# Optimization experiments

Hardware: AMD Instinct MI355X
Metric: run time of the kernel (lower is better)

The kernel has to match this reference:

```python
import jax, jax.numpy as jnp
import numpy as np

N_NODES = 20000
N_EDGES = 640000
IN_DIM = 128
HID_DIM = 256
N_CLASSES = 3
N_TYPES = 4
N_ASPECTS = 4096


def _type_aware_gcn(x, W_type, W_self, b, src, dst, etypes, n_nodes):
    # Per-node, per-type transforms: [N, T, H]
    xt = jnp.einsum('nd,tdh->nth', x, W_type)
    # Per-edge message: transform of source node under the edge's type. [E, H]
    msg = xt[src, etypes]
    # Degree-normalized scatter-sum into destination nodes.
    agg = jax.ops.segment_sum(msg, dst, num_segments=n_nodes)
    deg = jax.ops.segment_sum(jnp.ones((src.shape[0],), dtype=x.dtype), dst,
                              num_segments=n_nodes)
    agg = agg / jnp.clip(deg, 1.0)[:, None]
    # Self-loop transform + bias.
    return agg + x @ W_self + b


def setup_inputs() -> dict:
    key = jax.random.key(0)
    ks = jax.random.split(key, 12)
    features = jax.random.normal(ks[0], (N_NODES, IN_DIM), dtype=jnp.float32)
    edge_index = jax.random.randint(ks[1], (2, N_EDGES), 0, N_NODES)
    edge_types = jax.random.randint(ks[2], (N_EDGES,), 0, N_TYPES)
    aspect_indices = jax.random.randint(ks[3], (N_ASPECTS,), 0, N_NODES)
    s1 = 1.0 / np.sqrt(IN_DIM)
    s2 = 1.0 / np.sqrt(HID_DIM)
    W_type1 = jax.random.uniform(ks[4], (N_TYPES, IN_DIM, HID_DIM), minval=-s1, maxval=s1)
    W_self1 = jax.random.uniform(ks[5], (IN_DIM, HID_DIM), minval=-s1, maxval=s1)
    b1 = jnp.zeros((HID_DIM,), dtype=jnp.float32)
    W_type2 = jax.random.uniform(ks[6], (N_TYPES, HID_DIM, HID_DIM), minval=-s2, maxval=s2)
    W_self2 = jax.random.uniform(ks[7], (HID_DIM, HID_DIM), minval=-s2, maxval=s2)
    b2 = jnp.zeros((HID_DIM,), dtype=jnp.float32)
    W_cls = jax.random.uniform(ks[8], (HID_DIM, N_CLASSES), minval=-s2, maxval=s2)
    b_cls = jnp.zeros((N_CLASSES,), dtype=jnp.float32)
    return {
        'features': features,
        'W_type1': W_type1, 'W_self1': W_self1, 'b1': b1,
        'W_type2': W_type2, 'W_self2': W_self2, 'b2': b2,
        'W_cls': W_cls, 'b_cls': b_cls,
        'edge_index': edge_index,
        'edge_types': edge_types,
        'aspect_indices': aspect_indices,
    }


def reference(features, W_type1, W_self1, b1, W_type2, W_self2, b2,
              W_cls, b_cls, edge_index, edge_types, aspect_indices):
    n = features.shape[0]
    src, dst = edge_index[0], edge_index[1]
    h = _type_aware_gcn(features, W_type1, W_self1, b1, src, dst, edge_types, n)
    h = jax.nn.relu(h)
    # dropout: eval mode -> identity
    h = _type_aware_gcn(h, W_type2, W_self2, b2, src, dst, edge_types, n)
    aspect_embeddings = h[aspect_indices]            # [A, H]
    logits = aspect_embeddings @ W_cls + b_cls       # [A, C]
    return logits
```

## Files before the change

### kernel.cpp

```cpp
#include <hip/hip_runtime.h>

#define N_NODES   20000
#define N_EDGES   640000
#define IN_DIM    128
#define HID_DIM   256
#define N_TYPES   4
#define N_ASPECTS 4096
#define NT4       (N_NODES * N_TYPES)
#define NBUCK     157
#define BCAP      5120
#define CHUNK     2560

typedef __bf16 v8bf __attribute__((ext_vector_type(8)));
typedef float  f32x4 __attribute__((ext_vector_type(4)));
typedef float  v2f   __attribute__((ext_vector_type(2)));

static __device__ __forceinline__ float bf2f(unsigned short u) {
    return __builtin_bit_cast(float, ((unsigned int)u) << 16);
}
static __device__ __forceinline__ float bflo(unsigned int u) {
    return __builtin_bit_cast(float, u << 16);
}
static __device__ __forceinline__ float bfhi(unsigned int u) {
    return __builtin_bit_cast(float, u & 0xffff0000u);
}
static __device__ __forceinline__ unsigned short f2bf(float f) {
    unsigned int u = __builtin_bit_cast(unsigned int, f);
    u += 0x7fffu + ((u >> 16) & 1u);
    return (unsigned short)(u >> 16);
}

static __device__ __forceinline__ int local_flag(const unsigned short* w, int* red) {
    int tid = threadIdx.x;
    int c = 0;
    for (int i = tid; i < 1024; i += 256) {
        unsigned hb = (w[i] >> 8) & 0x7f;
        c += (hb >= 0x39 && hb <= 0x3D) ? 1 : 0;
    }
#pragma unroll
    for (int off = 32; off >= 1; off >>= 1) c += __shfl_down(c, off);
    if ((tid & 63) == 0) red[tid >> 6] = c;
    __syncthreads();
    int tot = red[0] + red[1] + red[2] + red[3];
    __syncthreads();
    return (tot >= 768) ? 1 : 0;
}

__global__ __launch_bounds__(256) void prepA_kernel(
        const void* __restrict__ x,
        const void* __restrict__ Ws1, const void* __restrict__ Wt1,
        const void* __restrict__ Ws2, const void* __restrict__ Wt2,
        const int* __restrict__ ei, const int* __restrict__ et,
        unsigned short* __restrict__ xc,
        unsigned int* __restrict__ xc8,
        unsigned short* __restrict__ WT1,
        unsigned short* __restrict__ WT2,
        int* __restrict__ bucket_cursor,
        unsigned int* __restrict__ breg,
        int* __restrict__ flag) {
    __shared__ __align__(16) char smem[14336];
    int b = blockIdx.x, tid = threadIdx.x;
    if (b < 250) {
        unsigned int* ord = (unsigned int*)smem;
        int* hist  = (int*)(smem + 10240);
        int* start = hist + NBUCK;
        int* cur   = start + NBUCK;
        int* gbase = cur + NBUCK;
        int* sbuf  = gbase + NBUCK;
        int e0 = b * CHUNK;
        for (int i = tid; i < NBUCK; i += 256) hist[i] = 0;
        __syncthreads();
        unsigned int pk[10];
        int bk[10];
#pragma unroll
        for (int r = 0; r < 10; r++) {
            int e = e0 + r * 256 + tid;
            int s = __builtin_nontemporal_load(ei + e);
            int d = __builtin_nontemporal_load(ei + N_EDGES + e);
            int t = __builtin_nontemporal_load(et + e);
            pk[r] = (unsigned int)s | ((unsigned int)t << 15) | ((unsigned int)d << 17);
            bk[r] = d >> 7;
            atomicAdd(&hist[bk[r]], 1);
        }
        __syncthreads();
        int v = (tid < NBUCK) ? hist[tid] : 0;
        sbuf[tid] = v;
        __syncthreads();
        for (int o = 1; o < 256; o <<= 1) {
            int t = (tid >= o) ? sbuf[tid - o] : 0;
            __syncthreads();
            sbuf[tid] += t;
            __syncthreads();
        }
        if (tid < NBUCK) { start[tid] = sbuf[tid] - v; cur[tid] = sbuf[tid] - v; }
        __syncthreads();
#pragma unroll
        for (int r = 0; r < 10; r++) {
            int p = atomicAdd(&cur[bk[r]], 1);
            ord[p] = pk[r];
        }
        __syncthreads();
        for (int bb = tid; bb < NBUCK; bb += 256)
            if (hist[bb] > 0) gbase[bb] = atomicAdd(bucket_cursor + bb, hist[bb]);
        __syncthreads();
        for (int p = tid; p < CHUNK; p += 256) {
            unsigned int e = ord[p];
            int bb = (int)(e >> 24);
            int gp = gbase[bb] + (p - start[bb]);
            if (gp < BCAP)
                __builtin_nontemporal_store(e, breg + (size_t)bb * BCAP + gp);
        }
    } else if (b < 1500) {
        int bf = local_flag((const unsigned short*)Ws1, (int*)smem);
        int idx = (b - 250) * 256 + tid;
        float f[8];
        if (bf) {
            uint4 v = reinterpret_cast<const uint4*>(x)[idx];
            reinterpret_cast<uint4*>(xc)[idx] = v;
            f[0] = bflo(v.x); f[1] = bfhi(v.x);
            f[2] = bflo(v.y); f[3] = bfhi(v.y);
            f[4] = bflo(v.z); f[5] = bfhi(v.z);
            f[6] = bflo(v.w); f[7] = bfhi(v.w);
        } else {
            const float* xf = reinterpret_cast<const float*>(x) + (size_t)idx * 8;
            unsigned short r[8] __attribute__((aligned(16)));
#pragma unroll
            for (int j = 0; j < 8; j++) { f[j] = xf[j]; r[j] = f2bf(xf[j]); }
            reinterpret_cast<uint4*>(xc)[idx] = *reinterpret_cast<const uint4*>(r);
        }
        int lo = 0, hi = 0;
        lo = __builtin_amdgcn_cvt_pk_fp8_f32(f[0], f[1], lo, false);
        lo = __builtin_amdgcn_cvt_pk_fp8_f32(f[2], f[3], lo, true);
        hi = __builtin_amdgcn_cvt_pk_fp8_f32(f[4], f[5], hi, false);
        hi = __builtin_amdgcn_cvt_pk_fp8_f32(f[6], f[7], hi, true);
        xc8[idx * 2]     = (unsigned int)lo;
        xc8[idx * 2 + 1] = (unsigned int)hi;
    } else if (b < 2140) {
        int bf = local_flag((const unsigned short*)Ws1, (int*)smem);
        int idx = (b - 1500) * 256 + tid;
        int n = idx / 640, k = idx - n * 640;
        const void* p = (k < 128) ? Ws1 : Wt1;
        size_t src = (k < 128) ? ((size_t)k * 256 + n) : ((size_t)(k - 128) * 256 + n);
        WT1[idx] = bf ? ((const unsigned short*)p)[src] : f2bf(((const float*)p)[src]);
    } else if (b < 3420) {
        int bf = local_flag((const unsigned short*)Ws1, (int*)smem);
        int idx = (b - 2140) * 256 + tid;
        int n = idx / 1280, k = idx - n * 1280;
        const void* p = (k < 256) ? Ws2 : Wt2;
        size_t src = (k < 256) ? ((size_t)k * 256 + n) : ((size_t)(k - 256) * 256 + n);
        WT2[idx] = bf ? ((const unsigned short*)p)[src] : f2bf(((const float*)p)[src]);
    } else {
        int bf = local_flag((const unsigned short*)Ws1, (int*)smem);
        if (tid == 0) *flag = bf;
    }
}

__global__ __launch_bounds__(256) void bucketB_kernel(
        const unsigned int* __restrict__ breg,
        const int* __restrict__ bucket_cursor,
        unsigned short* __restrict__ perm,
        int* __restrict__ offsets4) {
    __shared__ int cnt[512], off[512];
    __shared__ int buf[256], pscan[256];
    int b = blockIdx.x, tid = threadIdx.x;
    int cv = (tid < NBUCK) ? bucket_cursor[tid] : 0;
    if (cv > BCAP) cv = BCAP;
    buf[tid] = cv;
    __syncthreads();
    for (int o = 1; o < 256; o <<= 1) {
        int t = (tid >= o) ? buf[tid - o] : 0;
        __syncthreads();
        buf[tid] += t;
        __syncthreads();
    }
    int obase = (b > 0) ? buf[b - 1] : 0;
    if (b == 0 && tid == 0) offsets4[NT4] = buf[255];
    int Eb = bucket_cursor[b];
    if (Eb > BCAP) Eb = BCAP;
    for (int i = tid; i < 512; i += 256) cnt[i] = 0;
    __syncthreads();
    const unsigned int* reg = breg + (size_t)b * BCAP;
    for (int i = tid; i < Eb; i += 256) {
        unsigned int e = reg[i];
        int seg = (((e >> 17) & 127) << 2) | ((e >> 15) & 3);
        atomicAdd(&cnt[seg], 1);
    }
    __syncthreads();
    int pv = cnt[2 * tid] + cnt[2 * tid + 1];
    pscan[tid] = pv;
    __syncthreads();
    for (int o = 1; o < 256; o <<= 1) {
        int t = (tid >= o) ? pscan[tid - o] : 0;
        __syncthreads();
        pscan[tid] += t;
        __syncthreads();
    }
    int pexcl = pscan[tid] - pv;
    off[2 * tid]     = pexcl;
    off[2 * tid + 1] = pexcl + cnt[2 * tid];
    __syncthreads();
    for (int i = tid; i < 512; i += 256) {
        int node = b * 128 + (i >> 2);
        if (node < N_NODES) offsets4[node * 4 + (i & 3)] = obase + off[i];
    }
    __syncthreads();
    for (int i = tid; i < Eb; i += 256) {
        unsigned int e = reg[i];
        int seg = (((e >> 17) & 127) << 2) | ((e >> 15) & 3);
        int p = atomicAdd(&off[seg], 1);
        perm[obase + p] = (unsigned short)(e & 0x7fff);
    }
}

static __device__ __forceinline__ void acc8(uint2 x, float* a) {
    v2f p0 = __builtin_amdgcn_cvt_pk_f32_fp8((int)x.x, false);
    v2f p1 = __builtin_amdgcn_cvt_pk_f32_fp8((int)x.x, true);
    v2f p2 = __builtin_amdgcn_cvt_pk_f32_fp8((int)x.y, false);
    v2f p3 = __builtin_amdgcn_cvt_pk_f32_fp8((int)x.y, true);
    a[0] += p0.x; a[1] += p0.y;
    a[2] += p1.x; a[3] += p1.y;
    a[4] += p2.x; a[5] += p2.y;
    a[6] += p3.x; a[7] += p3.y;
}

template <int D>
__global__ __launch_bounds__(256) void agg8_kernel(
        const unsigned int* __restrict__ F8,
        const int* __restrict__ offs4,
        const unsigned short* __restrict__ perm,
        unsigned short* __restrict__ AG) {
    constexpr int G = D / 8;
    constexpr int SGN = 64 / G;
    int wave = threadIdx.x >> 6, lane = threadIdx.x & 63;
    int sg = lane / G;
    int gl = lane - sg * G;
    int sgid0   = (blockIdx.x * 4 + wave) * SGN + sg;
    int sstride = gridDim.x * 4 * SGN;
    for (int T = sgid0; T < NT4; T += sstride) {
        int n = T >> 2;
        int t = T & 3;
        int o0 = offs4[n * 4];
        int o4 = offs4[n * 4 + 4];
        int s0 = offs4[T];
        int s1 = offs4[T + 1];
        int deg = o4 - o0;
        float inv = 1.0f / (float)(deg > 1 ? deg : 1);
        float a[8];
#pragma unroll
        for (int v = 0; v < 8; v++) a[v] = 0.f;
        int j = s0;
        while (j < s1) {
            int m = s1 - j;
            if (m > G) m = G;
            int pw = (int)perm[j + ((gl < m) ? gl : 0)];
            for (int k = 0; k < m; k += 8) {
                uint2 x[8];
#pragma unroll
                for (int l = 0; l < 8; l++) {
                    int idx   = k + l;
                    int valid = (idx < m);
                    int src   = __shfl(pw, valid ? idx : (m - 1), G);
                    x[l] = *reinterpret_cast<const uint2*>(F8 + (size_t)src * (D / 4) + gl * 2);
                    unsigned msk = valid ? 0xffffffffu : 0u;
                    x[l].x &= msk; x[l].y &= msk;
                }
#pragma unroll
                for (int l = 0; l < 8; l++) acc8(x[l], a);
            }
            j += m;
        }
        unsigned short r[8] __attribute__((aligned(16)));
#pragma unroll
        for (int v = 0; v < 8; v++) r[v] = f2bf(a[v] * inv);
        *reinterpret_cast<uint4*>(AG + (size_t)n * (4 * D) + t * D + gl * 8) =
            *reinterpret_cast<const uint4*>(r);
    }
}

template <int D>
__global__ __launch_bounds__(256, 6) void gemm_kernel(
        const unsigned short* __restrict__ X,
        const unsigned short* __restrict__ AG,
        const unsigned short* __restrict__ BT,
        const void* __restrict__ bias,
        const int* __restrict__ flagp,
        unsigned short* __restrict__ C,
        unsigned char* __restrict__ C8,
        int M, int relu) {
    constexpr int K = 5 * D;
    constexpr int LDW = 72;
    __shared__ __align__(16) unsigned short As[64 * LDW];
    __shared__ __align__(16) unsigned short Bs[64 * LDW];
    int b = blockIdx.x;
    int mt = (b & 7) + 8 * (b >> 5);
    int nt = (b >> 3) & 3;
    int mtiles = (M + 63) >> 6;
    if (mt >= mtiles) return;
    int m0 = mt * 64;
    int n0 = nt * 64;
    int tid  = threadIdx.x;
    int wave = tid >> 6, lane = tid & 63;
    int wm = wave >> 1, wn = wave & 1;
    int quad = lane >> 4, l16 = lane & 15;

    f32x4 acc[2][2];
#pragma unroll
    for (int i = 0; i < 2; i++)
#pragma unroll
        for (int j = 0; j < 2; j++) acc[i][j] = (f32x4){0.f, 0.f, 0.f, 0.f};

    for (int k0 = 0; k0 < K; k0 += 64) {
        const unsigned short* base = (k0 < D) ? X : AG;
        int rs  = (k0 < D) ? D : 4 * D;
        int col = (k0 < D) ? k0 : (k0 - D);
#pragma unroll
        for (int cc = 0; cc < 2; cc++) {
            int c   = tid + cc * 256;
            int row = c >> 3;
            int c8  = c & 7;
            uint4 va = make_uint4(0u, 0u, 0u, 0u);
            int gr = m0 + row;
            if (gr < M)
                va = *reinterpret_cast<const uint4*>(base + (size_t)gr * rs + col + c8 * 8);
            *reinterpret_cast<uint4*>(&As[row * LDW + c8 * 8]) = va;
            uint4 vb = *reinterpret_cast<const uint4*>(BT + (size_t)(n0 + row) * K + k0 + c8 * 8);
            *reinterpret_cast<uint4*>(&Bs[row * LDW + c8 * 8]) = vb;
        }
        __syncthreads();
#pragma unroll
        for (int ks = 0; ks < 2; ks++) {
            v8bf af[2], bfr[2];
#pragma unroll
            for (int i = 0; i < 2; i++)
                af[i] = *reinterpret_cast<const v8bf*>(
                    &As[(wm * 32 + i * 16 + l16) * LDW + ks * 32 + quad * 8]);
#pragma unroll
            for (int j = 0; j < 2; j++)
                bfr[j] = *reinterpret_cast<const v8bf*>(
                    &Bs[(wn * 32 + j * 16 + l16) * LDW + ks * 32 + quad * 8]);
#pragma unroll
            for (int i = 0; i < 2; i++)
#pragma unroll
                for (int j = 0; j < 2; j++)
                    acc[i][j] = __builtin_amdgcn_mfma_f32_16x16x32_bf16(af[i], bfr[j], acc[i][j], 0, 0, 0);
        }
        __syncthreads();
    }
    int bf = *flagp;
#pragma unroll
    for (int i = 0; i < 2; i++) {
#pragma unroll
        for (int j = 0; j < 2; j++) {
            int col = n0 + wn * 32 + j * 16 + l16;
            float bv = bf ? bf2f(((const unsigned short*)bias)[col])
                          : ((const float*)bias)[col];
#pragma unroll
            for (int r = 0; r < 4; r++) {
                int row = m0 + wm * 32 + i * 16 + quad * 4 + r;
                if (row < M) {
                    float v = acc[i][j][r] + bv;
                    if (relu) v = fmaxf(v, 0.0f);
                    C[(size_t)row * 256 + col] = f2bf(v);
                    if (C8) {
                        int pk = __builtin_amdgcn_cvt_pk_fp8_f32(v, v, 0, false);
                        C8[(size_t)row * 256 + col] = (unsigned char)(pk & 0xff);
                    }
                }
            }
        }
    }
}

__global__ void cls_kernel(const unsigned short* __restrict__ h2,
                           const int* __restrict__ aidx,
                           const void* __restrict__ Wc,
                           const void* __restrict__ bc,
                           const int* __restrict__ flagp,
                           void* __restrict__ out) {
    int lin = blockIdx.x * blockDim.x + threadIdx.x;
    int a = lin >> 6, lane = lin & 63;
    if (a >= N_ASPECTS) return;
    int bf = *flagp;
    int node = aidx[a];
    uint2 v = *reinterpret_cast<const uint2*>(h2 + (size_t)node * 256 + lane * 4);
    float hv[4] = {bflo(v.x), bfhi(v.x), bflo(v.y), bfhi(v.y)};
    float a0 = 0.f, a1 = 0.f, a2 = 0.f;
#pragma unroll
    for (int r = 0; r < 4; r++) {
        int k = lane * 4 + r;
        float w0 = bf ? bf2f(((const unsigned short*)Wc)[k * 3 + 0]) : ((const float*)Wc)[k * 3 + 0];
        float w1 = bf ? bf2f(((const unsigned short*)Wc)[k * 3 + 1]) : ((const float*)Wc)[k * 3 + 1];
        float w2 = bf ? bf2f(((const unsigned short*)Wc)[k * 3 + 2]) : ((const float*)Wc)[k * 3 + 2];
        a0 += hv[r] * w0;
        a1 += hv[r] * w1;
        a2 += hv[r] * w2;
    }
#pragma unroll
    for (int off = 32; off >= 1; off >>= 1) {
        a0 += __shfl_down(a0, off);
        a1 += __shfl_down(a1, off);
        a2 += __shfl_down(a2, off);
    }
    if (lane == 0) {
        float b0 = bf ? bf2f(((const unsigned short*)bc)[0]) : ((const float*)bc)[0];
        float b1 = bf ? bf2f(((const unsigned short*)bc)[1]) : ((const float*)bc)[1];
        float b2 = bf ? bf2f(((const unsigned short*)bc)[2]) : ((const float*)bc)[2];
        if (bf) {
            unsigned short* o = (unsigned short*)out;
            o[a * 3 + 0] = f2bf(a0 + b0);
            o[a * 3 + 1] = f2bf(a1 + b1);
            o[a * 3 + 2] = f2bf(a2 + b2);
        } else {
            float* o = (float*)out;
            o[a * 3 + 0] = a0 + b0;
            o[a * 3 + 1] = a1 + b1;
            o[a * 3 + 2] = a2 + b2;
        }
    }
}

extern "C" void kernel_launch(void* const* d_in, const int* in_sizes, int n_in,
                              void* d_out, int out_size, void* d_ws, size_t ws_size,
                              hipStream_t stream) {
    const void* x   = d_in[0];
    const void* Wt1 = d_in[1];
    const void* Ws1 = d_in[2];
    const void* b1  = d_in[3];
    const void* Wt2 = d_in[4];
    const void* Ws2 = d_in[5];
    const void* b2  = d_in[6];
    const void* Wc  = d_in[7];
    const void* bc  = d_in[8];
    const int* ei = (const int*)d_in[9];
    const int* et = (const int*)d_in[10];
    const int* ai = (const int*)d_in[11];

    char* ws = (char*)d_ws;
    size_t off = 0;
    auto alloc = [&](size_t bytes) {
        void* p = ws + off;
        off += (bytes + 255) & ~(size_t)255;
        return p;
    };
    int*            flag          = (int*)alloc(4);
    int*            bucket_cursor = (int*)alloc((size_t)NBUCK * 4);
    int*            offsets4      = (int*)alloc((size_t)(NT4 + 1) * 4);
    unsigned int*   breg          = (unsigned int*)alloc((size_t)NBUCK * BCAP * 4);
    unsigned short* perm          = (unsigned short*)alloc((size_t)N_EDGES * 2);
    unsigned short* xc            = (unsigned short*)alloc((size_t)N_NODES * IN_DIM * 2);
    unsigned int*   xc8           = (unsigned int*)alloc((size_t)N_NODES * IN_DIM);
    unsigned short* AG            = (unsigned short*)alloc((size_t)N_NODES * 4 * HID_DIM * 2);
    unsigned short* h             = (unsigned short*)alloc((size_t)N_NODES * HID_DIM * 2);
    unsigned char*  h8            = (unsigned char*)alloc((size_t)N_NODES * HID_DIM);
    unsigned short* h2            = (unsigned short*)alloc((size_t)N_NODES * HID_DIM * 2);
    unsigned short* WT1           = (unsigned short*)alloc((size_t)640 * 256 * 2);
    unsigned short* WT2           = (unsigned short*)alloc((size_t)1280 * 256 * 2);

    hipMemsetAsync(bucket_cursor, 0, (size_t)NBUCK * 4, stream);
    prepA_kernel<<<3421, 256, 0, stream>>>(x, Ws1, Wt1, Ws2, Wt2, ei, et,
                                           xc, xc8, WT1, WT2, bucket_cursor, breg, flag);
    bucketB_kernel<<<NBUCK, 256, 0, stream>>>(breg, bucket_cursor, perm, offsets4);

    agg8_kernel<IN_DIM><<<4096, 256, 0, stream>>>(xc8, offsets4, perm, AG);
    gemm_kernel<IN_DIM><<<1280, 256, 0, stream>>>(xc, AG, WT1, b1, flag, h, h8, N_NODES, 1);
    agg8_kernel<HID_DIM><<<4096, 256, 0, stream>>>((const unsigned int*)h8, offsets4, perm, AG);
    gemm_kernel<HID_DIM><<<1280, 256, 0, stream>>>(h, AG, WT2, b2, flag, h2, nullptr, N_NODES, 0);
    cls_kernel<<<(N_ASPECTS * 64) / 256, 256, 0, stream>>>(h2, ai, Wc, bc, flag, d_out);
}
```

Baseline: 216.8 us.

## Double-buffer GEMM tiles with direct global-to-LDS async loads

Replaces the register-staged tile loads in the fused GEMM with global_load_lds direct-to-LDS copies into a double-buffered shared-memory layout, prefetching the next K step while MFMAs run on the current one. The LDS row padding is dropped, which allows the direct loads but may bring back LDS bank conflicts on the fragment reads. Out-of-range rows are clamped rather than zero-filled. The occupancy hint is also removed from the launch bounds. There is no explicit vmcnt wait before the barrier, so correctness depends on the compiler inserting the wait before __syncthreads.

```diff
diff --git a/kernel.cpp b/kernel.cpp
--- a/kernel.cpp
+++ b/kernel.cpp
@@ -28,6 +28,13 @@
     unsigned int u = __builtin_bit_cast(unsigned int, f);
     u += 0x7fffu + ((u >> 16) & 1u);
     return (unsigned short)(u >> 16);
+}
+
+static __device__ __forceinline__ void gload16(const unsigned short* g, unsigned short* l) {
+    __builtin_amdgcn_global_load_lds(
+        (const __attribute__((address_space(1))) void*)g,
+        (__attribute__((address_space(3))) void*)l,
+        16, 0, 0);
 }
 
 static __device__ __forceinline__ int local_flag(const unsigned short* w, int* red) {
@@ -278,7 +285,7 @@
 }
 
 template <int D>
-__global__ __launch_bounds__(256, 6) void gemm_kernel(
+__global__ __launch_bounds__(256) void gemm_kernel(
         const unsigned short* __restrict__ X,
         const unsigned short* __restrict__ AG,
         const unsigned short* __restrict__ BT,
@@ -288,9 +295,9 @@
         unsigned char* __restrict__ C8,
         int M, int relu) {
     constexpr int K = 5 * D;
-    constexpr int LDW = 72;
-    __shared__ __align__(16) unsigned short As[64 * LDW];
-    __shared__ __align__(16) unsigned short Bs[64 * LDW];
+    constexpr int NSTEP = K / 64;
+    __shared__ __align__(16) unsigned short As[2 * 64 * 64];
+    __shared__ __align__(16) unsigned short Bs[2 * 64 * 64];
     int b = blockIdx.x;
     int mt = (b & 7) + 8 * (b >> 5);
     int nt = (b >> 3) & 3;
@@ -309,35 +316,50 @@
 #pragma unroll
         for (int j = 0; j < 2; j++) acc[i][j] = (f32x4){0.f, 0.f, 0.f, 0.f};
 
-    for (int k0 = 0; k0 < K; k0 += 64) {
-        const unsigned short* base = (k0 < D) ? X : AG;
+    int srow = tid >> 3;
+    int sc8  = tid & 7;
+
+    auto stage = [&](int t, int buf) {
+        int k0 = t * 64;
+        const unsigned short* abase = (k0 < D) ? X : AG;
         int rs  = (k0 < D) ? D : 4 * D;
         int col = (k0 < D) ? k0 : (k0 - D);
-#pragma unroll
-        for (int cc = 0; cc < 2; cc++) {
-            int c   = tid + cc * 256;
-            int row = c >> 3;
-            int c8  = c & 7;
-            uint4 va = make_uint4(0u, 0u, 0u, 0u);
-            int gr = m0 + row;
-            if (gr < M)
-                va = *reinterpret_cast<const uint4*>(base + (size_t)gr * rs + col + c8 * 8);
-            *reinterpret_cast<uint4*>(&As[row * LDW + c8 * 8]) = va;
-            uint4 vb = *reinterpret_cast<const uint4*>(BT + (size_t)(n0 + row) * K + k0 + c8 * 8);
-            *reinterpret_cast<uint4*>(&Bs[row * LDW + c8 * 8]) = vb;
-        }
-        __syncthreads();
+        unsigned short* As_ = As + buf * (64 * 64);
+        unsigned short* Bs_ = Bs + buf * (64 * 64);
+#pragma unroll
+        for (int p = 0; p < 2; p++) {
+            int c   = p * 256 + tid;
+            int row = p * 32 + srow;
+            int gr  = m0 + row;
+            if (gr >= M) gr = M - 1;
+            gload16(abase + (size_t)gr * rs + col + sc8 * 8, As_ + c * 8);
+        }
+#pragma unroll
+        for (int p = 0; p < 2; p++) {
+            int c   = p * 256 + tid;
+            int row = p * 32 + srow;
+            gload16(BT + (size_t)(n0 + row) * K + k0 + sc8 * 8, Bs_ + c * 8);
+        }
+    };
+
+    stage(0, 0);
+    __syncthreads();
+    int cur = 0;
+    for (int t = 0; t < NSTEP; t++) {
+        if (t + 1 < NSTEP) stage(t + 1, cur ^ 1);
+        const unsigned short* As_ = As + cur * (64 * 64);
+        const unsigned short* Bs_ = Bs + cur * (64 * 64);
 #pragma unroll
         for (int ks = 0; ks < 2; ks++) {
             v8bf af[2], bfr[2];
 #pragma unroll
             for (int i = 0; i < 2; i++)
                 af[i] = *reinterpret_cast<const v8bf*>(
-                    &As[(wm * 32 + i * 16 + l16) * LDW + ks * 32 + quad * 8]);
+                    &As_[(wm * 32 + i * 16 + l16) * 64 + ks * 32 + quad * 8]);
 #pragma unroll
             for (int j = 0; j < 2; j++)
                 bfr[j] = *reinterpret_cast<const v8bf*>(
-                    &Bs[(wn * 32 + j * 16 + l16) * LDW + ks * 32 + quad * 8]);
+                    &Bs_[(wn * 32 + j * 16 + l16) * 64 + ks * 32 + quad * 8]);
 #pragma unroll
             for (int i = 0; i < 2; i++)
 #pragma unroll
@@ -345,6 +367,7 @@
                     acc[i][j] = __builtin_amdgcn_mfma_f32_16x16x32_bf16(af[i], bfr[j], acc[i][j], 0, 0, 0);
         }
         __syncthreads();
+        cur ^= 1;
     }
     int bf = *flagp;
 #pragma unroll
```

After: 229.6 us. +5.9%, slower.
